# Performance work log

Hardware: AMD Instinct MI355X
Metric: run time of the kernel (lower is better)

Reference implementation:

```python
import jax, jax.numpy as jnp
import numpy as np

EPS = 1e-3  # BatchNorm1d eps


def _fc_relu(x, W, b):
    return jax.nn.relu(x @ W + b)


def _fc_bn_relu(x, W, b, gamma, beta):
    # Linear -> BatchNorm1d (training mode: batch stats, biased var) -> ReLU
    h = x @ W + b
    m = jnp.mean(h, axis=0)
    v = jnp.var(h, axis=0)  # biased, matches torch BN normalization
    return jax.nn.relu((h - m) * jax.lax.rsqrt(v + EPS) * gamma + beta)


def _mmnet(img, tag, lat, lon, Wi, bi, gi, bti, Wt, bt, gt, btt, Wl, bl, gl, btl,
           W1, b1, W2, b2, W3, b3, W4, b4, W5, b5, W6, b6, W7, b7):
    img = _fc_bn_relu(img, Wi, bi, gi, bti)          # [B,300]
    tag = _fc_bn_relu(tag, Wt, bt, gt, btt)          # [B,300]
    loc = jnp.concatenate([lat, lon], axis=1)        # [B,2]
    loc = _fc_bn_relu(loc, Wl, bl, gl, btl)          # [B,10]
    x = jnp.concatenate([loc, img, tag], axis=1)     # [B,610]
    x = _fc_relu(x, W1, b1)                          # [B,2048]
    x = _fc_relu(x, W2, b2)                          # [B,2048]
    x = _fc_relu(x, W3, b3)                          # [B,1024]
    x = _fc_relu(x, W4, b4)                          # [B,1024]
    x = _fc_relu(x, W5, b5)                          # [B,512]
    x = _fc_relu(x, W6, b6)                          # [B,512]
    return x @ W7 + b7                               # [B,1]


def setup_inputs() -> dict:
    key = jax.random.key(0)
    ks = iter(jax.random.split(key, 64))
    B = 16384
    inp = {}
    inp['img_p'] = jax.random.normal(next(ks), (B, 300), jnp.float32)
    inp['tag_p'] = jax.random.normal(next(ks), (B, 300), jnp.float32)
    inp['lat_p'] = jax.random.uniform(next(ks), (B, 1), jnp.float32)
    inp['lon_p'] = jax.random.uniform(next(ks), (B, 1), jnp.float32)
    inp['img_n'] = jax.random.normal(next(ks), (B, 300), jnp.float32)
    inp['tag_n'] = jax.random.normal(next(ks), (B, 300), jnp.float32)
    inp['lat_n'] = jax.random.uniform(next(ks), (B, 1), jnp.float32)
    inp['lon_n'] = jax.random.uniform(next(ks), (B, 1), jnp.float32)
    inp['margin'] = 1

    def lin(din, dout):
        # matches l.weight.data.normal_(0, 0.01), bias zero; stored [din,dout]
        return (jax.random.normal(next(ks), (din, dout), jnp.float32) * 0.01,
                jnp.zeros((dout,), jnp.float32))

    inp['Wi'], inp['bi'] = lin(300, 300)
    inp['gi'], inp['bti'] = jnp.ones((300,), jnp.float32), jnp.zeros((300,), jnp.float32)
    inp['Wt'], inp['bt'] = lin(300, 300)
    inp['gt'], inp['btt'] = jnp.ones((300,), jnp.float32), jnp.zeros((300,), jnp.float32)
    inp['Wl'], inp['bl'] = lin(2, 10)
    inp['gl'], inp['btl'] = jnp.ones((10,), jnp.float32), jnp.zeros((10,), jnp.float32)
    inp['W1'], inp['b1'] = lin(610, 2048)
    inp['W2'], inp['b2'] = lin(2048, 2048)
    inp['W3'], inp['b3'] = lin(2048, 1024)
    inp['W4'], inp['b4'] = lin(1024, 1024)
    inp['W5'], inp['b5'] = lin(1024, 512)
    inp['W6'], inp['b6'] = lin(512, 512)
    inp['W7'], inp['b7'] = lin(512, 1)
    return inp


def reference(img_p, tag_p, lat_p, lon_p, img_n, tag_n, lat_n, lon_n,
              Wi, bi, gi, bti, Wt, bt, gt, btt, Wl, bl, gl, btl,
              W1, b1, W2, b2, W3, b3, W4, b4, W5, b5, W6, b6, W7, b7, margin):
    params = (Wi, bi, gi, bti, Wt, bt, gt, btt, Wl, bl, gl, btl,
              W1, b1, W2, b2, W3, b3, W4, b4, W5, b5, W6, b6, W7, b7)
    score_p = _mmnet(img_p, tag_p, lat_p, lon_p, *params)  # [B,1]
    score_n = _mmnet(img_n, tag_n, lat_n, lon_n, *params)  # [B,1]
    # vectorized replacement of the per-element python loop
    correct = jnp.sum((score_p - score_n)[:, 0] > margin).astype(jnp.int32)
    return score_p, score_n, correct
```

## Files before the change

kernel.cpp:

```cpp
#include <hip/hip_runtime.h>
#include <hip/hip_fp16.h>

typedef _Float16 half8 __attribute__((ext_vector_type(8)));
typedef float f32x16 __attribute__((ext_vector_type(16)));

#define B_ROWS 16384
#define M_ALL  32768

__device__ __forceinline__ void glds16(void* lds, const void* g) {
  __builtin_amdgcn_global_load_lds(
      (const __attribute__((address_space(1))) unsigned int*)g,
      (__attribute__((address_space(3))) unsigned int*)lds, 16, 0, 0);
}

template<int EPI>
__global__ __launch_bounds__(256, 2)
void gemm128(const _Float16* __restrict__ A, const _Float16* __restrict__ Bt,
             const float* __restrict__ bias, _Float16* __restrict__ Cout,
             int M, int N, int K) {
  __shared__ _Float16 As[128 * 64];
  __shared__ _Float16 Bs[128 * 64];
  const int tid = threadIdx.x;
  const int w = tid >> 6, l = tid & 63;
  const int bm = blockIdx.y << 7, bn = blockIdx.x << 7;
  const int wm = (w >> 1) << 6, wn = (w & 1) << 6;
  const int l31 = l & 31, g5 = l >> 5, l7 = l & 7, l3 = l >> 3;

  f32x16 acc[2][2];
#pragma unroll
  for (int i = 0; i < 2; ++i)
#pragma unroll
    for (int j = 0; j < 2; ++j)
#pragma unroll
      for (int r = 0; r < 16; ++r) acc[i][j][r] = 0.f;

  const int schunk = (l7 ^ l3) * 8;
  const int srow = w * 32 + l3;

  for (int kt = 0; kt < K; kt += 64) {
#pragma unroll
    for (int c = 0; c < 4; ++c)
      glds16(&As[w * 2048 + c * 512],
             A + (size_t)(bm + srow + c * 8) * K + kt + schunk);
#pragma unroll
    for (int c = 0; c < 4; ++c)
      glds16(&Bs[w * 2048 + c * 512],
             Bt + (size_t)(bn + srow + c * 8) * K + kt + schunk);
    __syncthreads();
#pragma unroll
    for (int ks = 0; ks < 4; ++ks) {
      const int p0 = (((ks * 2 + g5) ^ l7)) * 8;
      half8 af[2], bf[2];
#pragma unroll
      for (int i = 0; i < 2; ++i)
        af[i] = *(const half8*)&As[(wm + i * 32 + l31) * 64 + p0];
#pragma unroll
      for (int i = 0; i < 2; ++i)
        bf[i] = *(const half8*)&Bs[(wn + i * 32 + l31) * 64 + p0];
#pragma unroll
      for (int i = 0; i < 2; ++i)
#pragma unroll
        for (int j = 0; j < 2; ++j)
          acc[i][j] = __builtin_amdgcn_mfma_f32_32x32x16_f16(af[i], bf[j], acc[i][j], 0, 0, 0);
    }
    __syncthreads();
  }

#pragma unroll
  for (int i = 0; i < 2; ++i)
#pragma unroll
    for (int j = 0; j < 2; ++j) {
      const int col = bn + wn + j * 32 + l31;
      float bv = 0.f;
      if (EPI == 1) bv = bias[col];
#pragma unroll
      for (int r = 0; r < 16; ++r) {
        const int row = bm + wm + i * 32 + (r & 3) + 8 * (r >> 2) + 4 * g5;
        const float v = acc[i][j][r] + bv;
        Cout[(size_t)row * N + col] = (_Float16)(EPI == 1 ? fmaxf(v, 0.f) : v);
      }
    }
}

__global__ void tpose_pad(const float* __restrict__ src, _Float16* __restrict__ dst,
                          int Ks, int Ns, int Kd, int Nd) {
  __shared__ float t[32][33];
  const int k0 = blockIdx.x * 32, n0 = blockIdx.y * 32;
  const int tx = threadIdx.x & 31, ty = threadIdx.x >> 5;
#pragma unroll
  for (int i = ty; i < 32; i += 8) {
    const int k = k0 + i, n = n0 + tx;
    t[i][tx] = (k < Ks && n < Ns) ? src[(size_t)k * Ns + n] : 0.f;
  }
  __syncthreads();
#pragma unroll
  for (int i = ty; i < 32; i += 8)
    dst[(size_t)(n0 + i) * Kd + (k0 + tx)] = (_Float16)t[tx][i];
}

__global__ void cvt_in_k(const float* __restrict__ xp, const float* __restrict__ xn,
                         _Float16* __restrict__ X, int C, int Cp) {
  const size_t total = (size_t)M_ALL * Cp;
  const size_t stride = (size_t)gridDim.x * blockDim.x;
  for (size_t idx = (size_t)blockIdx.x * blockDim.x + threadIdx.x; idx < total; idx += stride) {
    const int r = (int)(idx / Cp);
    const int c = (int)(idx - (size_t)r * Cp);
    float v = 0.f;
    if (c < C) v = (r < B_ROWS) ? xp[(size_t)r * C + c] : xn[(size_t)(r - B_ROWS) * C + c];
    X[idx] = (_Float16)v;
  }
}

__global__ void stats_k(const _Float16* __restrict__ h, float* __restrict__ sums, int ldh, int C) {
  const int half = blockIdx.y;
  const int nr = B_ROWS / gridDim.x;
  const int r0 = half * B_ROWS + blockIdx.x * nr;
  for (int c = threadIdx.x; c < C; c += blockDim.x) {
    float s = 0.f, q = 0.f;
    for (int r = 0; r < nr; ++r) {
      const float v = (float)h[(size_t)(r0 + r) * ldh + c];
      s += v; q += v * v;
    }
    atomicAdd(&sums[(half * 2 + 0) * 384 + c], s);
    atomicAdd(&sums[(half * 2 + 1) * 384 + c], q);
  }
}

__global__ void bn_apply_k(const _Float16* __restrict__ h, const float* __restrict__ sums,
                           const float* __restrict__ gamma, const float* __restrict__ beta,
                           _Float16* __restrict__ X1, int coff) {
  const size_t total = (size_t)M_ALL * 300;
  const size_t stride = (size_t)gridDim.x * blockDim.x;
  for (size_t idx = (size_t)blockIdx.x * blockDim.x + threadIdx.x; idx < total; idx += stride) {
    const int r = (int)(idx / 300);
    const int c = (int)(idx - (size_t)r * 300);
    const int hf = r >> 14;
    const float mean = sums[(hf * 2 + 0) * 384 + c] * (1.f / 16384.f);
    const float ms   = sums[(hf * 2 + 1) * 384 + c] * (1.f / 16384.f);
    const float inv = rsqrtf(ms - mean * mean + 1e-3f) * gamma[c];
    const float y = ((float)h[(size_t)r * 384 + c] - mean) * inv + beta[c];
    X1[(size_t)r * 640 + coff + c] = (_Float16)fmaxf(y, 0.f);
  }
}

__global__ void loc_k(const float* __restrict__ lat_p, const float* __restrict__ lon_p,
                      const float* __restrict__ lat_n, const float* __restrict__ lon_n,
                      const float* __restrict__ Wl, const float* __restrict__ gl,
                      const float* __restrict__ btl, _Float16* __restrict__ X1) {
  const int j = blockIdx.x, half = blockIdx.y;
  const float* lat = half ? lat_n : lat_p;
  const float* lon = half ? lon_n : lon_p;
  const float w0 = Wl[j], w1 = Wl[10 + j];
  const int t = threadIdx.x;
  float s = 0.f, q = 0.f;
  for (int r = t; r < B_ROWS; r += 256) {
    const float v = lat[r] * w0 + lon[r] * w1;
    s += v; q += v * v;
  }
  __shared__ float rs[256], rq[256];
  rs[t] = s; rq[t] = q;
  __syncthreads();
  for (int o = 128; o; o >>= 1) {
    if (t < o) { rs[t] += rs[t + o]; rq[t] += rq[t + o]; }
    __syncthreads();
  }
  const float mean = rs[0] * (1.f / 16384.f);
  const float var = rq[0] * (1.f / 16384.f) - mean * mean;
  const float inv = rsqrtf(var + 1e-3f) * gl[j];
  const float bb = btl[j];
  for (int r = t; r < B_ROWS; r += 256) {
    const float v = lat[r] * w0 + lon[r] * w1;
    const float y = (v - mean) * inv + bb;
    X1[(size_t)(half * B_ROWS + r) * 640 + j] = (_Float16)fmaxf(y, 0.f);
  }
}

__global__ void scores_k(const _Float16* __restrict__ Y, const float* __restrict__ w7,
                         const float* __restrict__ b7, float* __restrict__ out) {
  const int row = blockIdx.x * 4 + (threadIdx.x >> 6);
  const int l = threadIdx.x & 63;
  const half8 v = *(const half8*)(Y + (size_t)row * 512 + l * 8);
  float s = 0.f;
#pragma unroll
  for (int j = 0; j < 8; ++j) s += (float)v[j] * w7[l * 8 + j];
#pragma unroll
  for (int o = 32; o; o >>= 1) s += __shfl_down(s, o);
  if (l == 0) out[row] = s + b7[0];
}

__global__ void correct_k(const float* __restrict__ sc, const int* __restrict__ mg,
                          float* __restrict__ dst) {
  __shared__ int red[256];
  const int t = threadIdx.x;
  const float m = (float)(*mg);
  int c = 0;
  for (int i = t; i < B_ROWS; i += 256)
    c += (sc[i] - sc[B_ROWS + i]) > m ? 1 : 0;
  red[t] = c;
  __syncthreads();
  for (int o = 128; o; o >>= 1) {
    if (t < o) red[t] += red[t + o];
    __syncthreads();
  }
  if (t == 0) dst[0] = (float)red[0];
}

extern "C" void kernel_launch(void* const* d_in, const int* in_sizes, int n_in,
                              void* d_out, int out_size, void* d_ws, size_t ws_size,
                              hipStream_t stream) {
  const float* img_p = (const float*)d_in[0];
  const float* tag_p = (const float*)d_in[1];
  const float* lat_p = (const float*)d_in[2];
  const float* lon_p = (const float*)d_in[3];
  const float* img_n = (const float*)d_in[4];
  const float* tag_n = (const float*)d_in[5];
  const float* lat_n = (const float*)d_in[6];
  const float* lon_n = (const float*)d_in[7];
  const int*   margin = (const int*)d_in[8];
  const float* Wi = (const float*)d_in[9];
  const float* gi = (const float*)d_in[11];
  const float* bti = (const float*)d_in[12];
  const float* Wt = (const float*)d_in[13];
  const float* gt = (const float*)d_in[15];
  const float* btt = (const float*)d_in[16];
  const float* Wl = (const float*)d_in[17];
  const float* gl = (const float*)d_in[19];
  const float* btl = (const float*)d_in[20];
  const float* W1 = (const float*)d_in[21]; const float* b1 = (const float*)d_in[22];
  const float* W2 = (const float*)d_in[23]; const float* b2 = (const float*)d_in[24];
  const float* W3 = (const float*)d_in[25]; const float* b3 = (const float*)d_in[26];
  const float* W4 = (const float*)d_in[27]; const float* b4 = (const float*)d_in[28];
  const float* W5 = (const float*)d_in[29]; const float* b5 = (const float*)d_in[30];
  const float* W6 = (const float*)d_in[31]; const float* b6 = (const float*)d_in[32];
  const float* W7 = (const float*)d_in[33]; const float* b7 = (const float*)d_in[34];
  float* out = (float*)d_out;

  char* ws = (char*)d_ws;
  size_t off = 0;
  auto alloc = [&](size_t bytes) -> void* {
    void* p = ws + off;
    off += (bytes + 255) & ~(size_t)255;
    return p;
  };
  _Float16* WiT = (_Float16*)alloc((size_t)384 * 320 * 2);
  _Float16* WtT = (_Float16*)alloc((size_t)384 * 320 * 2);
  _Float16* W1T = (_Float16*)alloc((size_t)2048 * 640 * 2);
  _Float16* W2T = (_Float16*)alloc((size_t)2048 * 2048 * 2);
  _Float16* W3T = (_Float16*)alloc((size_t)1024 * 2048 * 2);
  _Float16* W4T = (_Float16*)alloc((size_t)1024 * 1024 * 2);
  _Float16* W5T = (_Float16*)alloc((size_t)512 * 1024 * 2);
  _Float16* W6T = (_Float16*)alloc((size_t)512 * 512 * 2);
  float* sbuf = (float*)alloc((size_t)2 * 4 * 384 * 4);
  _Float16* X1 = (_Float16*)alloc((size_t)M_ALL * 640 * 2);

  const size_t persist = off;
  const size_t avail = ws_size > persist ? ws_size - persist : 0;
  int CR = 4096;
  if (avail >= (size_t)2 * 32768 * 2048 * 2) CR = 32768;
  else if (avail >= (size_t)2 * 16384 * 2048 * 2) CR = 16384;
  else if (avail >= (size_t)2 * 8192 * 2048 * 2) CR = 8192;
  _Float16* Ya = (_Float16*)(ws + persist);
  _Float16* Yb = Ya + (size_t)CR * 2048;
  _Float16* Ximg = Ya;
  _Float16* hbuf = (_Float16*)((char*)Ya + (size_t)M_ALL * 320 * 2);

  (void)hipMemsetAsync(X1, 0, (size_t)M_ALL * 640 * 2, stream);
  (void)hipMemsetAsync(sbuf, 0, (size_t)2 * 4 * 384 * 4, stream);

  tpose_pad<<<dim3(10, 12), 256, 0, stream>>>(Wi, WiT, 300, 300, 320, 384);
  tpose_pad<<<dim3(10, 12), 256, 0, stream>>>(Wt, WtT, 300, 300, 320, 384);
  tpose_pad<<<dim3(20, 64), 256, 0, stream>>>(W1, W1T, 610, 2048, 640, 2048);
  tpose_pad<<<dim3(64, 64), 256, 0, stream>>>(W2, W2T, 2048, 2048, 2048, 2048);
  tpose_pad<<<dim3(64, 32), 256, 0, stream>>>(W3, W3T, 2048, 1024, 2048, 1024);
  tpose_pad<<<dim3(32, 32), 256, 0, stream>>>(W4, W4T, 1024, 1024, 1024, 1024);
  tpose_pad<<<dim3(32, 16), 256, 0, stream>>>(W5, W5T, 1024, 512, 1024, 512);
  tpose_pad<<<dim3(16, 16), 256, 0, stream>>>(W6, W6T, 512, 512, 512, 512);

  cvt_in_k<<<2048, 256, 0, stream>>>(img_p, img_n, Ximg, 300, 320);
  gemm128<2><<<dim3(3, 256), 256, 0, stream>>>(Ximg, WiT, nullptr, hbuf, M_ALL, 384, 320);
  stats_k<<<dim3(128, 2), 256, 0, stream>>>(hbuf, sbuf, 384, 300);
  bn_apply_k<<<2048, 256, 0, stream>>>(hbuf, sbuf, gi, bti, X1, 10);
  cvt_in_k<<<2048, 256, 0, stream>>>(tag_p, tag_n, Ximg, 300, 320);
  gemm128<2><<<dim3(3, 256), 256, 0, stream>>>(Ximg, WtT, nullptr, hbuf, M_ALL, 384, 320);
  stats_k<<<dim3(128, 2), 256, 0, stream>>>(hbuf, sbuf + 4 * 384, 384, 300);
  bn_apply_k<<<2048, 256, 0, stream>>>(hbuf, sbuf + 4 * 384, gt, btt, X1, 310);
  loc_k<<<dim3(10, 2), 256, 0, stream>>>(lat_p, lon_p, lat_n, lon_n, Wl, gl, btl, X1);

  for (int c0 = 0; c0 < M_ALL; c0 += CR) {
    const int rb = CR / 128;
    const _Float16* Xc = X1 + (size_t)c0 * 640;
    gemm128<1><<<dim3(16, rb), 256, 0, stream>>>(Xc, W1T, b1, Ya, CR, 2048, 640);
    gemm128<1><<<dim3(16, rb), 256, 0, stream>>>(Ya, W2T, b2, Yb, CR, 2048, 2048);
    gemm128<1><<<dim3(8, rb), 256, 0, stream>>>(Yb, W3T, b3, Ya, CR, 1024, 2048);
    gemm128<1><<<dim3(8, rb), 256, 0, stream>>>(Ya, W4T, b4, Yb, CR, 1024, 1024);
    gemm128<1><<<dim3(4, rb), 256, 0, stream>>>(Yb, W5T, b5, Ya, CR, 512, 1024);
    gemm128<1><<<dim3(4, rb), 256, 0, stream>>>(Ya, W6T, b6, Yb, CR, 512, 512);
    scores_k<<<CR / 4, 256, 0, stream>>>(Yb, W7, b7, out + c0);
  }

  correct_k<<<1, 256, 0, stream>>>(out, margin, out + 32768);
}
```

Baseline: 1.078 ms.

## Add 256x256-tile double-buffered GEMM kernel for the four largest MLP layers

Introduces a 512-thread gemm256 kernel with 256x256 output tiles, XOR-swizzled LDS layout, double-buffered global_load_lds prefetch, and setprio around MFMA bursts. It replaces gemm128 for layers 1-4, which carry most of the FLOPs. The aim is more data reuse per LDS load and better overlap of loads with MFMA. The cost is lower occupancy (one block per CU), larger LDS use, and fewer blocks per launch, which could underfill the GPU for small chunk sizes.

```diff
diff --git a/kernel.cpp b/kernel.cpp
--- a/kernel.cpp
+++ b/kernel.cpp
@@ -78,6 +78,102 @@
         const int row = bm + wm + i * 32 + (r & 3) + 8 * (r >> 2) + 4 * g5;
         const float v = acc[i][j][r] + bv;
         Cout[(size_t)row * N + col] = (_Float16)(EPI == 1 ? fmaxf(v, 0.f) : v);
+      }
+    }
+}
+
+__global__ __launch_bounds__(512, 1)
+void gemm256(const _Float16* __restrict__ A, const _Float16* __restrict__ Bt,
+             const float* __restrict__ bias, _Float16* __restrict__ Cout,
+             int M, int N, int K) {
+  __shared__ _Float16 smem[4 * 256 * 64];
+  const int tid = threadIdx.x;
+  const int w = tid >> 6, l = tid & 63;
+  const int bm = blockIdx.y << 8, bn = blockIdx.x << 8;
+  const int wm = w >> 2, wn = w & 3;
+  const int l31 = l & 31, g5 = l >> 5, l7 = l & 7, l3 = l >> 3;
+
+  f32x16 acc[4][2];
+#pragma unroll
+  for (int i = 0; i < 4; ++i)
+#pragma unroll
+    for (int j = 0; j < 2; ++j)
+#pragma unroll
+      for (int r = 0; r < 16; ++r) acc[i][j][r] = 0.f;
+
+  const int schunk = (l7 ^ l3) * 8;
+  const _Float16* aSrc = A + (size_t)(bm + w * 32 + l3) * K + schunk;
+  const _Float16* bSrc = Bt + (size_t)(bn + w * 32 + l3) * K + schunk;
+  const int NT = K >> 6;
+
+  auto stage = [&](int buf, int t) {
+    _Float16* as = smem + buf * 16384;
+    _Float16* bs = smem + 32768 + buf * 16384;
+    const size_t ko = (size_t)t * 64;
+#pragma unroll
+    for (int c = 0; c < 4; ++c)
+      glds16(as + (w * 32 + c * 8) * 64, aSrc + (size_t)c * 8 * K + ko);
+#pragma unroll
+    for (int c = 0; c < 4; ++c)
+      glds16(bs + (w * 32 + c * 8) * 64, bSrc + (size_t)c * 8 * K + ko);
+  };
+
+  stage(0, 0);
+  stage(1, 1);
+  asm volatile("s_waitcnt vmcnt(8)" ::: "memory");
+  __builtin_amdgcn_s_barrier();
+
+  half8 bf[2][4];
+  for (int t = 0; t < NT; ++t) {
+    const _Float16* as = smem + (t & 1) * 16384;
+    const _Float16* bs = smem + 32768 + (t & 1) * 16384;
+#pragma unroll
+    for (int p = 0; p < 4; ++p) {
+      half8 af[2][4];
+#pragma unroll
+      for (int i = 0; i < 2; ++i)
+#pragma unroll
+        for (int ks = 0; ks < 4; ++ks)
+          af[i][ks] = *(const half8*)(as + (wm * 128 + (p * 2 + i) * 32 + l31) * 64
+                                         + ((ks * 2 + g5) ^ l7) * 8);
+      if (p == 0) {
+#pragma unroll
+        for (int j = 0; j < 2; ++j)
+#pragma unroll
+          for (int ks = 0; ks < 4; ++ks)
+            bf[j][ks] = *(const half8*)(bs + (wn * 64 + j * 32 + l31) * 64
+                                           + ((ks * 2 + g5) ^ l7) * 8);
+      }
+      __builtin_amdgcn_s_barrier();
+      asm volatile("s_waitcnt lgkmcnt(0)" ::: "memory");
+      __builtin_amdgcn_sched_barrier(0);
+      __builtin_amdgcn_s_setprio(1);
+#pragma unroll
+      for (int ks = 0; ks < 4; ++ks)
+#pragma unroll
+        for (int i = 0; i < 2; ++i)
+#pragma unroll
+          for (int j = 0; j < 2; ++j)
+            acc[p * 2 + i][j] = __builtin_amdgcn_mfma_f32_32x32x16_f16(
+                af[i][ks], bf[j][ks], acc[p * 2 + i][j], 0, 0, 0);
+      __builtin_amdgcn_s_setprio(0);
+      if (p < 3) __builtin_amdgcn_s_barrier();
+    }
+    asm volatile("s_waitcnt vmcnt(0)" ::: "memory");
+    __builtin_amdgcn_s_barrier();
+    if (t + 2 < NT) stage(t & 1, t + 2);
+  }
+
+#pragma unroll
+  for (int mi = 0; mi < 4; ++mi)
+#pragma unroll
+    for (int nj = 0; nj < 2; ++nj) {
+      const int col = bn + wn * 64 + nj * 32 + l31;
+      const float bv = bias[col];
+#pragma unroll
+      for (int r = 0; r < 16; ++r) {
+        const int row = bm + wm * 128 + mi * 32 + (r & 3) + 8 * (r >> 2) + 4 * g5;
+        Cout[(size_t)row * N + col] = (_Float16)fmaxf(acc[mi][nj][r] + bv, 0.f);
       }
     }
 }
@@ -287,12 +383,12 @@
   loc_k<<<dim3(10, 2), 256, 0, stream>>>(lat_p, lon_p, lat_n, lon_n, Wl, gl, btl, X1);
 
   for (int c0 = 0; c0 < M_ALL; c0 += CR) {
-    const int rb = CR / 128;
+    const int rb = CR / 128, rb2 = CR / 256;
     const _Float16* Xc = X1 + (size_t)c0 * 640;
-    gemm128<1><<<dim3(16, rb), 256, 0, stream>>>(Xc, W1T, b1, Ya, CR, 2048, 640);
-    gemm128<1><<<dim3(16, rb), 256, 0, stream>>>(Ya, W2T, b2, Yb, CR, 2048, 2048);
-    gemm128<1><<<dim3(8, rb), 256, 0, stream>>>(Yb, W3T, b3, Ya, CR, 1024, 2048);
-    gemm128<1><<<dim3(8, rb), 256, 0, stream>>>(Ya, W4T, b4, Yb, CR, 1024, 1024);
+    gemm256<<<dim3(8, rb2), 512, 0, stream>>>(Xc, W1T, b1, Ya, CR, 2048, 640);
+    gemm256<<<dim3(8, rb2), 512, 0, stream>>>(Ya, W2T, b2, Yb, CR, 2048, 2048);
+    gemm256<<<dim3(4, rb2), 512, 0, stream>>>(Yb, W3T, b3, Ya, CR, 1024, 2048);
+    gemm256<<<dim3(4, rb2), 512, 0, stream>>>(Ya, W4T, b4, Yb, CR, 1024, 1024);
     gemm128<1><<<dim3(4, rb), 256, 0, stream>>>(Yb, W5T, b5, Ya, CR, 512, 1024);
     gemm128<1><<<dim3(4, rb), 256, 0, stream>>>(Ya, W6T, b6, Yb, CR, 512, 512);
     scores_k<<<CR / 4, 256, 0, stream>>>(Yb, W7, b7, out + c0);
```

Result: faster. 1.035 ms (-4.0%).

## Add 256x256 ping-pong pipelined GEMM for the four largest MLP layers

Applied to the files above, without the earlier changes.

Adds a new 512-thread GEMM kernel with 256x256 output tiles, double-buffered LDS filled by direct global-to-LDS loads, and an XOR-swizzled layout. It interleaves loads with 16x16x32 MFMA groups under explicit waitcnt, barriers and setprio. Workgroup IDs are remapped so neighbouring tiles share operands. It replaces the 128x128 kernel for layers 1-4 to raise arithmetic intensity and overlap memory with compute. The cost is larger LDS and register use and fragile hand-written synchronisation; NI=K/128 assumes K is a multiple of 128, which 640 satisfies.

```diff
diff --git a/kernel.cpp b/kernel.cpp
--- a/kernel.cpp
+++ b/kernel.cpp
@@ -3,6 +3,7 @@
 
 typedef _Float16 half8 __attribute__((ext_vector_type(8)));
 typedef float f32x16 __attribute__((ext_vector_type(16)));
+typedef float f32x4 __attribute__((ext_vector_type(4)));
 
 #define B_ROWS 16384
 #define M_ALL  32768
@@ -80,6 +81,129 @@
         Cout[(size_t)row * N + col] = (_Float16)(EPI == 1 ? fmaxf(v, 0.f) : v);
       }
     }
+}
+
+#define BAR  __builtin_amdgcn_s_barrier()
+#define LGKM0 asm volatile("s_waitcnt lgkmcnt(0)" ::: "memory")
+#define LGKM8 asm volatile("s_waitcnt lgkmcnt(8)" ::: "memory")
+#define VM4  asm volatile("s_waitcnt vmcnt(4)" ::: "memory")
+#define VM0  asm volatile("s_waitcnt vmcnt(0)" ::: "memory")
+#define LDA(AS, MH) \
+  _Pragma("unroll") for (int mi_ = 0; mi_ < 4; ++mi_) { \
+    _Pragma("unroll") for (int t2_ = 0; t2_ < 2; ++t2_) \
+      a[mi_][t2_] = *(const half8*)((AS) + (wm * 128 + ((MH) * 4 + mi_) * 16 + l15) * 64 \
+                                       + ((t2_ * 4 + kg) ^ l7) * 8); }
+#define LDB(BS, NH, BR) \
+  _Pragma("unroll") for (int nj_ = 0; nj_ < 2; ++nj_) { \
+    _Pragma("unroll") for (int t2_ = 0; t2_ < 2; ++t2_) \
+      BR[nj_][t2_] = *(const half8*)((BS) + (wn * 64 + ((NH) * 2 + nj_) * 16 + l15) * 64 \
+                                        + ((t2_ * 4 + kg) ^ l7) * 8); }
+#define MFMA16(MH, NH, BR) do { \
+  __builtin_amdgcn_s_setprio(1); \
+  _Pragma("unroll") for (int t2_ = 0; t2_ < 2; ++t2_) \
+    _Pragma("unroll") for (int mi_ = 0; mi_ < 4; ++mi_) \
+      _Pragma("unroll") for (int nj_ = 0; nj_ < 2; ++nj_) \
+        acc[(MH) * 4 + mi_][(NH) * 2 + nj_] = __builtin_amdgcn_mfma_f32_16x16x32_f16( \
+            a[mi_][t2_], BR[nj_][t2_], acc[(MH) * 4 + mi_][(NH) * 2 + nj_], 0, 0, 0); \
+  __builtin_amdgcn_s_setprio(0); } while (0)
+
+__global__ __launch_bounds__(512, 2)
+void gemm256(const _Float16* __restrict__ A, const _Float16* __restrict__ Bt,
+             const float* __restrict__ bias, _Float16* __restrict__ Cout,
+             int M, int N, int K) {
+  __shared__ _Float16 smem[4 * 256 * 64];
+  const int tid = threadIdx.x;
+  const int w = tid >> 6, l = tid & 63;
+  const int nwg = gridDim.x * gridDim.y;
+  const int orig = blockIdx.y * gridDim.x + blockIdx.x;
+  const int wgid = (orig & 7) * (nwg >> 3) + (orig >> 3);
+  const int bx = wgid % gridDim.x, by = wgid / gridDim.x;
+  const int bm = by << 8, bn = bx << 8;
+  const int wm = w >> 2, wn = w & 3;
+  const int l15 = l & 15, kg = l >> 4, l7 = l & 7;
+
+  f32x4 acc[8][4];
+#pragma unroll
+  for (int i = 0; i < 8; ++i)
+#pragma unroll
+    for (int j = 0; j < 4; ++j)
+#pragma unroll
+      for (int r = 0; r < 4; ++r) acc[i][j][r] = 0.f;
+
+  const int srow = tid >> 3;
+  const int schunk = ((tid & 7) ^ (srow & 7)) * 8;
+  const _Float16* aBase = A + (size_t)(bm + srow) * K + schunk;
+  const _Float16* bBase = Bt + (size_t)(bn + srow) * K + schunk;
+  const int NT = K >> 6, NI = NT >> 1;
+
+  auto stA = [&](int buf, int h, int t) {
+    const _Float16* s = aBase + (size_t)(h * 128) * K + (size_t)t * 64;
+    _Float16* d = smem + buf * 16384 + h * 8192 + w * 512;
+    glds16(d, s);
+    glds16(d + 4096, s + (size_t)64 * K);
+  };
+  auto stB = [&](int buf, int h, int t) {
+    const _Float16* s = bBase + (size_t)(h * 128) * K + (size_t)t * 64;
+    _Float16* d = smem + 32768 + buf * 16384 + h * 8192 + w * 512;
+    glds16(d, s);
+    glds16(d + 4096, s + (size_t)64 * K);
+  };
+
+  stB(0, 0, 0); stA(0, 0, 0); stA(0, 1, 0); stB(0, 1, 0);
+  stB(1, 0, 1); stA(1, 0, 1);
+  VM4; BAR;
+
+  const _Float16* as0 = smem;
+  const _Float16* as1 = smem + 16384;
+  const _Float16* bs0 = smem + 32768;
+  const _Float16* bs1 = smem + 49152;
+
+  half8 a[4][2], b0r[2][2], b1r[2][2];
+
+  for (int i = 0; i < NI; ++i) {
+    const int t1 = 2 * i + 1, tn0 = 2 * i + 2, tn1 = 2 * i + 3;
+    const bool s0 = tn0 < NT, s1 = tn1 < NT;
+    LDA(as0, 0); LDB(bs0, 0, b0r);
+    stA(1, 1, t1);
+    LGKM8; BAR; LGKM0; MFMA16(0, 0, b0r); BAR;
+    LDB(bs0, 1, b1r);
+    stB(1, 1, t1);
+    BAR; LGKM0; MFMA16(0, 1, b1r); BAR;
+    LDA(as0, 1);
+    if (s0) stB(0, 0, tn0);
+    BAR; LGKM0; MFMA16(1, 1, b1r); BAR;
+    if (s0) stA(0, 0, tn0);
+    BAR; LGKM0; MFMA16(1, 0, b0r);
+    if (s0) { VM4; } else { VM0; }
+    BAR;
+    LDA(as1, 0); LDB(bs1, 0, b0r);
+    if (s0) stA(0, 1, tn0);
+    LGKM8; BAR; LGKM0; MFMA16(0, 0, b0r); BAR;
+    LDB(bs1, 1, b1r);
+    if (s0) stB(0, 1, tn0);
+    BAR; LGKM0; MFMA16(0, 1, b1r); BAR;
+    LDA(as1, 1);
+    if (s1) stB(1, 0, tn1);
+    BAR; LGKM0; MFMA16(1, 1, b1r); BAR;
+    if (s1) stA(1, 0, tn1);
+    BAR; LGKM0; MFMA16(1, 0, b0r);
+    if (s1) { VM4; }
+    BAR;
+  }
+
+#pragma unroll
+  for (int nj = 0; nj < 4; ++nj) {
+    const int col = bn + wn * 64 + nj * 16 + l15;
+    const float bv = bias[col];
+#pragma unroll
+    for (int mi = 0; mi < 8; ++mi) {
+#pragma unroll
+      for (int r = 0; r < 4; ++r) {
+        const int row = bm + wm * 128 + mi * 16 + (kg << 2) + r;
+        Cout[(size_t)row * N + col] = (_Float16)fmaxf(acc[mi][nj][r] + bv, 0.f);
+      }
+    }
+  }
 }
 
 __global__ void tpose_pad(const float* __restrict__ src, _Float16* __restrict__ dst,
@@ -287,12 +411,12 @@
   loc_k<<<dim3(10, 2), 256, 0, stream>>>(lat_p, lon_p, lat_n, lon_n, Wl, gl, btl, X1);
 
   for (int c0 = 0; c0 < M_ALL; c0 += CR) {
-    const int rb = CR / 128;
+    const int rb = CR / 128, rb2 = CR / 256;
     const _Float16* Xc = X1 + (size_t)c0 * 640;
-    gemm128<1><<<dim3(16, rb), 256, 0, stream>>>(Xc, W1T, b1, Ya, CR, 2048, 640);
-    gemm128<1><<<dim3(16, rb), 256, 0, stream>>>(Ya, W2T, b2, Yb, CR, 2048, 2048);
-    gemm128<1><<<dim3(8, rb), 256, 0, stream>>>(Yb, W3T, b3, Ya, CR, 1024, 2048);
-    gemm128<1><<<dim3(8, rb), 256, 0, stream>>>(Ya, W4T, b4, Yb, CR, 1024, 1024);
+    gemm256<<<dim3(8, rb2), 512, 0, stream>>>(Xc, W1T, b1, Ya, CR, 2048, 640);
+    gemm256<<<dim3(8, rb2), 512, 0, stream>>>(Ya, W2T, b2, Yb, CR, 2048, 2048);
+    gemm256<<<dim3(4, rb2), 512, 0, stream>>>(Yb, W3T, b3, Ya, CR, 1024, 2048);
+    gemm256<<<dim3(4, rb2), 512, 0, stream>>>(Ya, W4T, b4, Yb, CR, 1024, 1024);
     gemm128<1><<<dim3(4, rb), 256, 0, stream>>>(Yb, W5T, b5, Ya, CR, 512, 1024);
     gemm128<1><<<dim3(4, rb), 256, 0, stream>>>(Ya, W6T, b6, Yb, CR, 512, 512);
     scores_k<<<CR / 4, 256, 0, stream>>>(Yb, W7, b7, out + c0);
```

Result: faster. 951.4 us (-11.8%).
